# Optimization experiments

Measured on AMD Instinct MI355X. Metric: run time of the kernel, lower is better.

## Reference

```python
import jax, jax.numpy as jnp
import numpy as np

B, T, D = 128, 197, 768          # batch, tokens, model dim
HEADS, HID_PER_HEAD = 12, 64
H = HEADS * HID_PER_HEAD         # lstm hidden size (== D by construction)


def _block_mask(in_per_head, hid_per_head, head_num):
    """Block-diagonal mask replicated over the 4 LSTM gates (i,f,g,o)."""
    Ht = hid_per_head * head_num
    Dt = in_per_head * head_num
    m = np.zeros((4 * Ht, Dt), np.float32)
    for h in range(head_num):
        for g in range(4):
            r0 = g * Ht + h * hid_per_head
            m[r0:r0 + hid_per_head, h * in_per_head:(h + 1) * in_per_head] = 1.0
    return jnp.asarray(m)


def setup_inputs() -> dict:
    key = jax.random.key(0)
    ks = jax.random.split(key, 16)
    s = 1.0 / np.sqrt(H)  # pytorch LSTM init scale
    u = lambda k, shape: jax.random.uniform(k, shape, jnp.float32, -s, s)
    mask_ih = _block_mask(D // HEADS, HID_PER_HEAD, HEADS)   # [4H, D]
    mask_hh = _block_mask(HID_PER_HEAD, HID_PER_HEAD, HEADS)  # [4H, H]
    inp = {
        "x": jax.random.normal(ks[0], (B, T, D), jnp.float32),
        "pre_w": u(ks[1], (D, D)),
        "pre_b": u(ks[2], (D,)),
        "w_ih_f": u(ks[3], (4 * H, D)) * mask_ih,
        "w_hh_f": u(ks[4], (4 * H, H)) * mask_hh,
        "b_ih_f": u(ks[5], (4 * H,)),
        "b_hh_f": u(ks[6], (4 * H,)),
        "w_ih_r": u(ks[7], (4 * H, D)) * mask_ih,
        "w_hh_r": u(ks[8], (4 * H, H)) * mask_hh,
        "b_ih_r": u(ks[9], (4 * H,)),
        "b_hh_r": u(ks[10], (4 * H,)),
        "proj_w": u(ks[11], (D, 2 * H)),
        "proj_b": u(ks[12], (D,)),
    }
    return inp


def _lstm_dir(x, w_ih, w_hh, b_ih, b_hh, reverse):
    # Precompute input contribution for all timesteps: [B,T,4H]
    xg = jnp.einsum('btd,gd->btg', x, w_ih) + b_ih + b_hh
    xs = jnp.swapaxes(xg, 0, 1)  # [T,B,4H]
    Bn = x.shape[0]

    def step(carry, gx):
        h, c = carry
        gates = gx + h @ w_hh.T
        i, f, g, o = jnp.split(gates, 4, axis=-1)  # pytorch gate order i,f,g,o
        i = jax.nn.sigmoid(i)
        f = jax.nn.sigmoid(f)
        g = jnp.tanh(g)
        o = jax.nn.sigmoid(o)
        c = f * c + i * g
        h = o * jnp.tanh(c)
        return (h, c), h

    init = (jnp.zeros((Bn, w_hh.shape[1]), x.dtype),
            jnp.zeros((Bn, w_hh.shape[1]), x.dtype))
    _, hs = jax.lax.scan(step, init, xs, reverse=reverse)  # outputs aligned to input order
    return jnp.swapaxes(hs, 0, 1)  # [B,T,H]


def reference(x, pre_w, pre_b, w_ih_f, w_hh_f, b_ih_f, b_hh_f,
              w_ih_r, w_hh_r, b_ih_r, b_hh_r, proj_w, proj_b):
    x = x @ pre_w.T + pre_b                      # pre_proj
    hf = _lstm_dir(x, w_ih_f, w_hh_f, b_ih_f, b_hh_f, reverse=False)
    hr = _lstm_dir(x, w_ih_r, w_hh_r, b_ih_r, b_hh_r, reverse=True)
    lstm_out = jnp.concatenate([hf, hr], axis=-1)  # [B,T,2H]
    return lstm_out @ proj_w.T + proj_b            # proj -> [B,T,D]
```

## Files before the change

### kernel.cpp

```cpp
#include <hip/hip_runtime.h>
#include <stdint.h>

#define DEV __device__ __forceinline__

typedef __attribute__((ext_vector_type(8))) short short8;
typedef __attribute__((ext_vector_type(4))) float floatx4;

#define BATCH 128
#define TT    197
#define DD    768
#define NH    12
#define NROWS (BATCH*TT)
#define G4H   3072
#define MT    197
#define NT    6

DEV uint16_t f2bf(float f) {
    union { float f; uint32_t u; } v; v.f = f;
    uint32_t r = (v.u + 0x7FFF + ((v.u >> 16) & 1)) >> 16;
    return (uint16_t)r;
}

DEV floatx4 mfma16(short8 a, short8 b, floatx4 c) {
    return __builtin_amdgcn_mfma_f32_16x16x32_bf16(a, b, c, 0, 0, 0);
}

DEV float sigf(float x)   { return __builtin_amdgcn_rcpf(1.0f + __expf(-x)); }
DEV float tanhf_(float x) { return 1.0f - 2.0f * __builtin_amdgcn_rcpf(1.0f + __expf(2.0f * x)); }

DEV void async16(const uint16_t* g, uint16_t* l) {
    __builtin_amdgcn_global_load_lds(
        (const __attribute__((address_space(1))) unsigned int*)g,
        (__attribute__((address_space(3))) unsigned int*)l,
        16, 0, 0);
}

struct CvtArgs {
    const float* src[7];
    uint16_t*    dst[7];
    int          n4[7];
    int          nseg;
};

__global__ void cvt_multi(CvtArgs a) {
    int tid = blockIdx.x * blockDim.x + threadIdx.x;
    int stride = gridDim.x * blockDim.x;
    for (int s = 0; s < a.nseg; s++) {
        const float4* src = (const float4*)a.src[s];
        ushort4* dst = (ushort4*)a.dst[s];
        int n4 = a.n4[s];
        for (int i = tid; i < n4; i += stride) {
            float4 v = src[i];
            ushort4 o;
            o.x = f2bf(v.x); o.y = f2bf(v.y); o.z = f2bf(v.z); o.w = f2bf(v.w);
            dst[i] = o;
        }
    }
}

template<int STORE_BF16, int LAYOUT>
__global__ __launch_bounds__(256) void gemm128(
    const uint16_t* __restrict__ A,
    const uint16_t* __restrict__ Bw,
    const float*    __restrict__ bias,
    void*           __restrict__ C,
    int K, int Ntot)
{
    __shared__ __attribute__((aligned(16))) uint16_t As[2][8 * 512];
    __shared__ __attribute__((aligned(16))) uint16_t Bs[2][8 * 512];

    const int bid = blockIdx.x;
    const int c   = bid & 7;
    const int j   = bid >> 3;
    const int mt_ = c + 8 * (j / NT);
    const int nt_ = j % NT;
    if (mt_ >= MT) return;
    const int m0 = mt_ * 128;
    const int n0 = nt_ * 128;

    const int tid  = threadIdx.x;
    const int wv   = tid >> 6;
    const int lane = tid & 63;
    const int ln   = lane & 15;
    const int q    = lane >> 4;
    const int wm   = wv >> 1;
    const int wn   = wv & 1;

    floatx4 acc[4][4];
#pragma unroll
    for (int a = 0; a < 4; a++)
#pragma unroll
        for (int b = 0; b < 4; b++) acc[a][b] = (floatx4){0.f, 0.f, 0.f, 0.f};

    const uint16_t* gA0 = A  + (size_t)(m0 + (2*wv+0)*16 + ln) * K + q*8;
    const uint16_t* gA1 = A  + (size_t)(m0 + (2*wv+1)*16 + ln) * K + q*8;
    const uint16_t* gB0 = Bw + (size_t)(n0 + (2*wv+0)*16 + ln) * K + q*8;
    const uint16_t* gB1 = Bw + (size_t)(n0 + (2*wv+1)*16 + ln) * K + q*8;
    uint16_t* lA0h0 = &As[0][(2*wv+0)*512]; uint16_t* lA0h1 = &As[1][(2*wv+0)*512];
    uint16_t* lA1h0 = &As[0][(2*wv+1)*512]; uint16_t* lA1h1 = &As[1][(2*wv+1)*512];
    uint16_t* lB0h0 = &Bs[0][(2*wv+0)*512]; uint16_t* lB0h1 = &Bs[1][(2*wv+0)*512];
    uint16_t* lB1h0 = &Bs[0][(2*wv+1)*512]; uint16_t* lB1h1 = &Bs[1][(2*wv+1)*512];

    for (int k0 = 0; k0 < K; k0 += 64) {
        __syncthreads();
        async16(gA0 + k0,      lA0h0);
        async16(gA0 + k0 + 32, lA0h1);
        async16(gA1 + k0,      lA1h0);
        async16(gA1 + k0 + 32, lA1h1);
        async16(gB0 + k0,      lB0h0);
        async16(gB0 + k0 + 32, lB0h1);
        async16(gB1 + k0,      lB1h0);
        async16(gB1 + k0 + 32, lB1h1);
        __syncthreads();

#pragma unroll
        for (int h = 0; h < 2; h++) {
            short8 af[4], bf[4];
#pragma unroll
            for (int mt = 0; mt < 4; mt++)
                af[mt] = *(const short8*)&As[h][(wm*4 + mt)*512 + lane*8];
#pragma unroll
            for (int nt = 0; nt < 4; nt++)
                bf[nt] = *(const short8*)&Bs[h][(wn*4 + nt)*512 + lane*8];
#pragma unroll
            for (int mt = 0; mt < 4; mt++)
#pragma unroll
                for (int nt = 0; nt < 4; nt++)
                    acc[mt][nt] = mfma16(af[mt], bf[nt], acc[mt][nt]);
        }
    }

#pragma unroll
    for (int mt = 0; mt < 4; mt++)
#pragma unroll
        for (int nt = 0; nt < 4; nt++) {
            int n = n0 + (wn*4 + nt)*16 + ln;
            float bv = bias[n];
#pragma unroll
            for (int r = 0; r < 4; r++) {
                int m = m0 + (wm*4 + mt)*16 + q*4 + r;
                float val = acc[mt][nt][r] + bv;
                if (LAYOUT == 1) {
                    int b = m / 197; int t = m - b*197;
                    int head = n >> 6; int d = n & 63;
                    size_t off = ((size_t)(t*NH + head)*BATCH + b)*64 + d;
                    ((uint16_t*)C)[off] = f2bf(val);
                } else {
                    size_t off = (size_t)m * Ntot + n;
                    if (STORE_BF16) ((uint16_t*)C)[off] = f2bf(val);
                    else            ((float*)C)[off]    = val;
                }
            }
        }
}

__global__ __launch_bounds__(256) void lstm_fused(
    const uint16_t* __restrict__ pre,
    const uint16_t* __restrict__ wih_f, const uint16_t* __restrict__ whh_f,
    const uint16_t* __restrict__ wih_r, const uint16_t* __restrict__ whh_r,
    const float* __restrict__ bih_f, const float* __restrict__ bhh_f,
    const float* __restrict__ bih_r, const float* __restrict__ bhh_r,
    uint16_t* __restrict__ hout)
{
    __shared__ __attribute__((aligned(16))) uint16_t hbuf[2][16][72];

    const int tid  = threadIdx.x;
    const int wv   = tid >> 6;
    const int lane = tid & 63;
    const int ln   = lane & 15;
    const int q    = lane >> 4;
    const int b0   = blockIdx.x * 16;
    const int head = blockIdx.y;
    const int dir  = blockIdx.z;
    const int ub   = wv * 16;

    const uint16_t* wih = dir ? wih_r : wih_f;
    const uint16_t* whh = dir ? whh_r : whh_f;
    const float*    bih = dir ? bih_r : bih_f;
    const float*    bhh = dir ? bhh_r : bhh_f;

    short8 aih[4][2], ahh[4][2];
#pragma unroll
    for (int t = 0; t < 4; t++) {
        size_t row = (size_t)(t*768 + head*64 + ub + ln);
#pragma unroll
        for (int s = 0; s < 2; s++) {
            aih[t][s] = *(const short8*)(wih + row*768 + head*64 + s*32 + q*8);
            ahh[t][s] = *(const short8*)(whh + row*768 + head*64 + s*32 + q*8);
        }
    }
    float biasv[4][4];
#pragma unroll
    for (int t = 0; t < 4; t++)
#pragma unroll
        for (int r = 0; r < 4; r++) {
            int row = t*768 + head*64 + ub + q*4 + r;
            biasv[t][r] = bih[row] + bhh[row];
        }

    for (int i = tid; i < 2*16*72; i += 256) ((uint16_t*)hbuf)[i] = 0;
    float c[4] = {0.f, 0.f, 0.f, 0.f};
    __syncthreads();

    const uint16_t* xbase = pre + (size_t)head*BATCH*64 + (size_t)(b0 + ln)*64 + q*8;
    int t_cur = dir ? (TT - 1) : 0;
    const int tstep = dir ? -1 : 1;
    size_t xo = (size_t)t_cur * NH * BATCH * 64;
    short8 xv0 = *(const short8*)(xbase + xo);
    short8 xv1 = *(const short8*)(xbase + xo + 32);

    for (int step = 0; step < TT; step++) {
        short8 cx0 = xv0, cx1 = xv1;
        int t_next = t_cur + tstep;
        if (step + 1 < TT) {
            size_t xo2 = (size_t)t_next * NH * BATCH * 64;
            xv0 = *(const short8*)(xbase + xo2);
            xv1 = *(const short8*)(xbase + xo2 + 32);
        }
        const int pb = (step + 1) & 1;
        const int cb = step & 1;
        short8 hb0 = *(const short8*)&hbuf[pb][ln][0*32 + q*8];
        short8 hb1 = *(const short8*)&hbuf[pb][ln][1*32 + q*8];

        floatx4 acc[4];
#pragma unroll
        for (int t = 0; t < 4; t++)
            acc[t] = (floatx4){biasv[t][0], biasv[t][1], biasv[t][2], biasv[t][3]};
#pragma unroll
        for (int t = 0; t < 4; t++) {
            acc[t] = mfma16(aih[t][0], cx0, acc[t]);
            acc[t] = mfma16(ahh[t][0], hb0, acc[t]);
            acc[t] = mfma16(aih[t][1], cx1, acc[t]);
            acc[t] = mfma16(ahh[t][1], hb1, acc[t]);
        }

        union { uint16_t s[4]; uint2 v; } hp;
#pragma unroll
        for (int r = 0; r < 4; r++) {
            float ig = sigf(acc[0][r]);
            float fg = sigf(acc[1][r]);
            float gg = tanhf_(acc[2][r]);
            float og = sigf(acc[3][r]);
            c[r] = fg * c[r] + ig * gg;
            float hv = og * tanhf_(c[r]);
            hp.s[r] = f2bf(hv);
        }

        *(uint2*)&hbuf[cb][ln][ub + q*4] = hp.v;
        __syncthreads();

        {
            int bl = tid >> 4;
            int dw = tid & 15;
            uint2 v = *(const uint2*)&hbuf[cb][bl][dw*4];
            size_t off = ((size_t)(b0 + bl)*TT + t_cur) * 1536 + dir*768 + head*64 + dw*4;
            *(uint2*)(hout + off) = v;
        }
        t_cur = t_next;
    }
}

extern "C" void kernel_launch(void* const* d_in, const int* in_sizes, int n_in,
                              void* d_out, int out_size, void* d_ws, size_t ws_size,
                              hipStream_t stream) {
    (void)in_sizes; (void)n_in; (void)out_size; (void)ws_size;
    const float* x     = (const float*)d_in[0];
    const float* pre_w = (const float*)d_in[1];
    const float* pre_b = (const float*)d_in[2];
    const float* wihf  = (const float*)d_in[3];
    const float* whhf  = (const float*)d_in[4];
    const float* bihf  = (const float*)d_in[5];
    const float* bhhf  = (const float*)d_in[6];
    const float* wihr  = (const float*)d_in[7];
    const float* whhr  = (const float*)d_in[8];
    const float* bihr  = (const float*)d_in[9];
    const float* bhhr  = (const float*)d_in[10];
    const float* projw = (const float*)d_in[11];
    const float* projb = (const float*)d_in[12];
    float* out = (float*)d_out;

    uint16_t* W = (uint16_t*)d_ws;
    uint16_t* xb     = W; W += (size_t)NROWS * DD;
    uint16_t* bwpre  = W; W += (size_t)DD * DD;
    uint16_t* bwihf  = W; W += (size_t)G4H * DD;
    uint16_t* bwhhf  = W; W += (size_t)G4H * DD;
    uint16_t* bwihr  = W; W += (size_t)G4H * DD;
    uint16_t* bwhhr  = W; W += (size_t)G4H * DD;
    uint16_t* bwproj = W; W += (size_t)DD * 2 * DD;
    uint16_t* preb   = W; W += (size_t)NROWS * DD;
    uint16_t* houtb  = W; W += (size_t)NROWS * 2 * DD;

    CvtArgs ca;
    ca.src[0] = x;     ca.dst[0] = xb;     ca.n4[0] = (int)((size_t)NROWS * DD / 4);
    ca.src[1] = pre_w; ca.dst[1] = bwpre;  ca.n4[1] = DD * DD / 4;
    ca.src[2] = wihf;  ca.dst[2] = bwihf;  ca.n4[2] = G4H * DD / 4;
    ca.src[3] = whhf;  ca.dst[3] = bwhhf;  ca.n4[3] = G4H * DD / 4;
    ca.src[4] = wihr;  ca.dst[4] = bwihr;  ca.n4[4] = G4H * DD / 4;
    ca.src[5] = whhr;  ca.dst[5] = bwhhr;  ca.n4[5] = G4H * DD / 4;
    ca.src[6] = projw; ca.dst[6] = bwproj; ca.n4[6] = DD * 2 * DD / 4;
    ca.nseg = 7;
    hipLaunchKernelGGL(cvt_multi, dim3(1024), dim3(256), 0, stream, ca);

    const int RPX = (MT + 7) / 8;
    const int GBLK = 8 * RPX * NT;

    hipLaunchKernelGGL((gemm128<1, 1>), dim3(GBLK), dim3(256), 0, stream,
                       xb, bwpre, pre_b, (void*)preb, DD, DD);
    hipLaunchKernelGGL(lstm_fused, dim3(8, 12, 2), dim3(256), 0, stream,
                       preb, bwihf, bwhhf, bwihr, bwhhr,
                       bihf, bhhf, bihr, bhhr, houtb);
    hipLaunchKernelGGL((gemm128<0, 0>), dim3(GBLK), dim3(256), 0, stream,
                       houtb, bwproj, projb, (void*)out, 2 * DD, DD);
}
```

Measured before the change: 516.0 us.

## Triple-buffer GEMM LDS tiles with async prefetch two stages ahead

```diff
diff --git a/kernel.cpp b/kernel.cpp
--- a/kernel.cpp
+++ b/kernel.cpp
@@ -34,6 +34,8 @@
         (__attribute__((address_space(3))) unsigned int*)l,
         16, 0, 0);
 }
+
+#define CFENCE() asm volatile("" ::: "memory")
 
 struct CvtArgs {
     const float* src[7];
@@ -59,15 +61,16 @@
 }
 
 template<int STORE_BF16, int LAYOUT>
-__global__ __launch_bounds__(256) void gemm128(
+__global__ __launch_bounds__(256) void gemm128p(
     const uint16_t* __restrict__ A,
     const uint16_t* __restrict__ Bw,
     const float*    __restrict__ bias,
     void*           __restrict__ C,
     int K, int Ntot)
 {
-    __shared__ __attribute__((aligned(16))) uint16_t As[2][8 * 512];
-    __shared__ __attribute__((aligned(16))) uint16_t Bs[2][8 * 512];
+    __shared__ __attribute__((aligned(16))) uint16_t As[3][4096];
+    __shared__ __attribute__((aligned(16))) uint16_t Bs[3][4096];
+    __shared__ __attribute__((aligned(16))) uint16_t Dump[512];
 
     const int bid = blockIdx.x;
     const int c   = bid & 7;
@@ -96,39 +99,53 @@
     const uint16_t* gA1 = A  + (size_t)(m0 + (2*wv+1)*16 + ln) * K + q*8;
     const uint16_t* gB0 = Bw + (size_t)(n0 + (2*wv+0)*16 + ln) * K + q*8;
     const uint16_t* gB1 = Bw + (size_t)(n0 + (2*wv+1)*16 + ln) * K + q*8;
-    uint16_t* lA0h0 = &As[0][(2*wv+0)*512]; uint16_t* lA0h1 = &As[1][(2*wv+0)*512];
-    uint16_t* lA1h0 = &As[0][(2*wv+1)*512]; uint16_t* lA1h1 = &As[1][(2*wv+1)*512];
-    uint16_t* lB0h0 = &Bs[0][(2*wv+0)*512]; uint16_t* lB0h1 = &Bs[1][(2*wv+0)*512];
-    uint16_t* lB1h0 = &Bs[0][(2*wv+1)*512]; uint16_t* lB1h1 = &Bs[1][(2*wv+1)*512];
-
-    for (int k0 = 0; k0 < K; k0 += 64) {
-        __syncthreads();
-        async16(gA0 + k0,      lA0h0);
-        async16(gA0 + k0 + 32, lA0h1);
-        async16(gA1 + k0,      lA1h0);
-        async16(gA1 + k0 + 32, lA1h1);
-        async16(gB0 + k0,      lB0h0);
-        async16(gB0 + k0 + 32, lB0h1);
-        async16(gB1 + k0,      lB1h0);
-        async16(gB1 + k0 + 32, lB1h1);
-        __syncthreads();
-
-#pragma unroll
-        for (int h = 0; h < 2; h++) {
+
+    const int NI = K >> 5;
+
+    auto stage = [&](int kiter, int buf) {
+        int k0 = kiter * 32;
+        const bool ok = k0 < K;
+        if (!ok) k0 = 0;
+        uint16_t* a0 = ok ? &As[buf][(2*wv+0)*512] : Dump;
+        uint16_t* a1 = ok ? &As[buf][(2*wv+1)*512] : Dump;
+        uint16_t* b0 = ok ? &Bs[buf][(2*wv+0)*512] : Dump;
+        uint16_t* b1 = ok ? &Bs[buf][(2*wv+1)*512] : Dump;
+        async16(gA0 + k0, a0);
+        async16(gA1 + k0, a1);
+        async16(gB0 + k0, b0);
+        async16(gB1 + k0, b1);
+    };
+
+    stage(0, 0); stage(1, 1); stage(2, 2);
+
+    for (int i = 0; i < NI; i += 3) {
+#pragma unroll
+        for (int u = 0; u < 3; u++) {
+            CFENCE();
+            __builtin_amdgcn_s_waitcnt(0x0F78);
+            __builtin_amdgcn_s_barrier();
+            CFENCE();
+
             short8 af[4], bf[4];
 #pragma unroll
             for (int mt = 0; mt < 4; mt++)
-                af[mt] = *(const short8*)&As[h][(wm*4 + mt)*512 + lane*8];
+                af[mt] = *(const short8*)&As[u][(wm*4 + mt)*512 + lane*8];
 #pragma unroll
             for (int nt = 0; nt < 4; nt++)
-                bf[nt] = *(const short8*)&Bs[h][(wn*4 + nt)*512 + lane*8];
+                bf[nt] = *(const short8*)&Bs[u][(wn*4 + nt)*512 + lane*8];
 #pragma unroll
             for (int mt = 0; mt < 4; mt++)
 #pragma unroll
                 for (int nt = 0; nt < 4; nt++)
                     acc[mt][nt] = mfma16(af[mt], bf[nt], acc[mt][nt]);
+
+            CFENCE();
+            __builtin_amdgcn_s_barrier();
+            CFENCE();
+            stage(i + u + 3, u);
         }
     }
+    __builtin_amdgcn_s_waitcnt(0x0F70);
 
 #pragma unroll
     for (int mt = 0; mt < 4; mt++)
@@ -304,11 +321,11 @@
     const int RPX = (MT + 7) / 8;
     const int GBLK = 8 * RPX * NT;
 
-    hipLaunchKernelGGL((gemm128<1, 1>), dim3(GBLK), dim3(256), 0, stream,
+    hipLaunchKernelGGL((gemm128p<1, 1>), dim3(GBLK), dim3(256), 0, stream,
                        xb, bwpre, pre_b, (void*)preb, DD, DD);
     hipLaunchKernelGGL(lstm_fused, dim3(8, 12, 2), dim3(256), 0, stream,
                        preb, bwihf, bwhhf, bwihr, bwhhr,
                        bihf, bhhf, bihr, bhhr, houtb);
-    hipLaunchKernelGGL((gemm128<0, 0>), dim3(GBLK), dim3(256), 0, stream,
+    hipLaunchKernelGGL((gemm128p<0, 0>), dim3(GBLK), dim3(256), 0, stream,
                        houtb, bwproj, projb, (void*)out, 2 * DD, DD);
 }
```

New measurement: 495.7 us. -3.9%, faster.
